# Optimization experiments

Hardware: AMD Instinct MI355X
Metric: run time of the kernel (lower is better)

## Reference

```python
import jax, jax.numpy as jnp
import numpy as np

N_NODES, N_EDGES, N_GRAPHS = 500000, 8000000, 4096
IN_SIZE, HIDDEN, OUT_SIZE = 11, 16, 4
FEAT = IN_SIZE + 7  # 18; also the (buggy) truncated sequence length in the original


def setup_inputs() -> dict:
    key = jax.random.key(0)
    ks = jax.random.split(key, 10)
    x = jax.random.normal(ks[0], (N_NODES, IN_SIZE), dtype=jnp.float32)
    edge_index = jax.random.randint(ks[1], (2, N_EDGES), 0, N_NODES)
    edge_attr = jax.random.randint(ks[2], (N_EDGES,), 0, 7)
    batch = jnp.sort(jax.random.randint(ks[3], (N_EDGES,), 0, N_GRAPHS))
    s = 0.1
    W_ih = jax.random.normal(ks[4], (4 * HIDDEN, FEAT), jnp.float32) * s
    W_hh = jax.random.normal(ks[5], (4 * HIDDEN, HIDDEN), jnp.float32) * s
    b_ih = jax.random.normal(ks[6], (4 * HIDDEN,), jnp.float32) * s
    b_hh = jax.random.normal(ks[7], (4 * HIDDEN,), jnp.float32) * s
    W_fc = jax.random.normal(ks[8], (OUT_SIZE, HIDDEN), jnp.float32) * s
    b_fc = jax.random.normal(ks[9], (OUT_SIZE,), jnp.float32) * s
    return {"x": x, "W_ih": W_ih, "W_hh": W_hh, "b_ih": b_ih, "b_hh": b_hh,
            "W_fc": W_fc, "b_fc": b_fc, "edge_index": edge_index,
            "edge_attr": edge_attr, "batch": batch, "num_graphs": N_GRAPHS}


def _forward(x, W_ih, W_hh, b_ih, b_hh, W_fc, b_fc, edge_index, edge_attr, batch, num_graphs):
    E = edge_index.shape[1]
    # Per-edge gather: node_value = x[n1] + x[n2], concat one-hot edge type (width 7)
    feat = jnp.concatenate(
        [x[edge_index[0]] + x[edge_index[1]],
         jax.nn.one_hot(edge_attr, 7, dtype=x.dtype)], axis=1)  # [E, FEAT]
    # Position of edge j within its graph: j - index of first edge of that graph
    first = jnp.searchsorted(batch, jnp.arange(num_graphs))  # [B]
    pos = jnp.arange(E) - first[batch]                        # [E], >= 0 (batch sorted)
    # Faithful to original bug: sequences truncated to first FEAT (=18) timesteps.
    # Out-of-range positions dropped by scatter mode='drop'.
    seq = jnp.zeros((num_graphs, FEAT, FEAT), x.dtype).at[batch, pos].set(feat, mode='drop')
    # Single-layer LSTM (torch gate order i, f, g, o), batch_first
    bias = b_ih + b_hh

    def step(carry, xt):
        h, c = carry
        gates = xt @ W_ih.T + h @ W_hh.T + bias  # [B, 4H]
        i, f, g, o = jnp.split(gates, 4, axis=-1)
        c = jax.nn.sigmoid(f) * c + jax.nn.sigmoid(i) * jnp.tanh(g)
        h = jax.nn.sigmoid(o) * jnp.tanh(c)
        return (h, c), None

    h0 = jnp.zeros((num_graphs, HIDDEN), x.dtype)
    (h, c), _ = jax.lax.scan(step, (h0, h0), jnp.swapaxes(seq, 0, 1))  # [T,B,F] scan
    # fc applied then last timestep taken -> equals fc(h_last)
    return h @ W_fc.T + b_fc  # [B, OUT_SIZE]


def reference(x, W_ih, W_hh, b_ih, b_hh, W_fc, b_fc, edge_index, edge_attr, batch, num_graphs):
    return _forward(x, W_ih, W_hh, b_ih, b_hh, W_fc, b_fc, edge_index, edge_attr, batch, num_graphs)
```

## Files before the change

kernel.cpp:

```cpp
#include <hip/hip_runtime.h>

#define IN_SIZE 11
#define HID 16
#define FEAT 18
#define TSTEPS 18

__device__ __forceinline__ float fast_rcp(float v) { return __builtin_amdgcn_rcpf(v); }

__device__ __forceinline__ float rl(float v, int lane) {
    return __int_as_float(__builtin_amdgcn_readlane(__float_as_int(v), lane));
}

extern "C" __global__ __launch_bounds__(256, 4)
void tgnn_lstm_fused(const float* __restrict__ x,
                     const float* __restrict__ W_ih,
                     const float* __restrict__ W_hh,
                     const float* __restrict__ b_ih,
                     const float* __restrict__ b_hh,
                     const float* __restrict__ W_fc,
                     const float* __restrict__ b_fc,
                     const int* __restrict__ edge_index,
                     const int* __restrict__ edge_attr,
                     const int* __restrict__ batch,
                     float* __restrict__ out,
                     int E, int B)
{
    const int wl  = threadIdx.x & 63;
    const int g   = (blockIdx.x * blockDim.x + threadIdx.x) >> 6;
    const int u   = wl & 15;
    const int r   = wl >> 4;
    const int row = wl;

    float wih[IN_SIZE], whh[HID];
#pragma unroll
    for (int k = 0; k < IN_SIZE; ++k) wih[k] = W_ih[row * FEAT + k];
#pragma unroll
    for (int v = 0; v < HID; ++v) whh[v] = W_hh[row * HID + v];
    const float bias = b_ih[row] + b_hh[row];
    const float wfc  = W_fc[row];
    const float bfc  = b_fc[r];

    const int tgt1 = g, tgt2 = g + 1;
    int lo1 = 0, hi1 = E, lo2 = 0, hi2 = E;
    while ((hi1 - lo1) > 64 || (hi2 - lo2) > 64) {
        const unsigned n1r = (unsigned)(hi1 - lo1);
        const unsigned n2r = (unsigned)(hi2 - lo2);
        const int p1 = lo1 + (int)((n1r * (unsigned)wl) >> 6);
        const int p2 = lo2 + (int)((n2r * (unsigned)wl) >> 6);
        const int b1 = batch[p1];
        const int b2 = batch[p2];
        const int c1 = __popcll(__ballot(b1 < tgt1));
        const int c2 = __popcll(__ballot(b2 < tgt2));
        const int nlo1 = c1 ? (lo1 + (int)((n1r * (unsigned)(c1 - 1)) >> 6) + 1) : lo1;
        const int nhi1 = (c1 < 64) ? (lo1 + (int)((n1r * (unsigned)c1) >> 6)) : hi1;
        const int nlo2 = c2 ? (lo2 + (int)((n2r * (unsigned)(c2 - 1)) >> 6) + 1) : lo2;
        const int nhi2 = (c2 < 64) ? (lo2 + (int)((n2r * (unsigned)c2) >> 6)) : hi2;
        lo1 = nlo1; hi1 = nhi1; lo2 = nlo2; hi2 = nhi2;
    }
    {
        const int n1r = hi1 - lo1, n2r = hi2 - lo2;
        int p1 = lo1 + ((wl < n1r) ? wl : 0);
        int p2 = lo2 + ((wl < n2r) ? wl : 0);
        if (p1 > E - 1) p1 = E - 1;
        if (p2 > E - 1) p2 = E - 1;
        const int b1 = batch[p1];
        const int b2 = batch[p2];
        lo1 += __popcll(__ballot((wl < n1r) && (b1 < tgt1)));
        lo2 += __popcll(__ballot((wl < n2r) && (b2 < tgt2)));
    }
    const int first = lo1;
    int cnt = lo2 - first;
    cnt = (cnt < 0) ? 0 : ((cnt > TSTEPS) ? TSTEPS : cnt);

    int n1 = 0, n2 = 0, ea = 0;
    if (wl < TSTEPS) {
        int j = first + wl;
        if (j > E - 1) j = E - 1;
        n1 = edge_index[j];
        n2 = edge_index[E + j];
        ea = edge_attr[j];
    }
    float f[IN_SIZE];
    {
        const float* xa = x + (long)n1 * IN_SIZE;
        const float* xb = x + (long)n2 * IN_SIZE;
#pragma unroll
        for (int k = 0; k < IN_SIZE; ++k) f[k] = xa[k] + xb[k];
    }
    if (wl >= cnt) {
#pragma unroll
        for (int k = 0; k < IN_SIZE; ++k) f[k] = 0.0f;
    }

    float ain[TSTEPS];
#pragma unroll
    for (int t = 0; t < TSTEPS; ++t) {
        const int eat = __builtin_amdgcn_readlane(ea, t);
        const float w1 = W_ih[row * FEAT + IN_SIZE + eat];
        float a = bias + ((t < cnt) ? w1 : 0.0f);
#pragma unroll
        for (int k = 0; k < IN_SIZE; ++k)
            a = fmaf(rl(f[k], t), wih[k], a);
        ain[t] = a;
    }

    const float sa = (r == 2) ? -2.0f : -1.0f;
    const float ma = (r == 2) ?  2.0f :  1.0f;
    const float oa = (r == 2) ? -1.0f :  0.0f;

    float h = 0.0f, c = 0.0f;
#pragma unroll
    for (int t = 0; t < TSTEPS; ++t) {
        float a;
        if (t == 0) {
            a = ain[0];
        } else {
            float A0 = ain[t], A1 = 0.0f, A2 = 0.0f, A3 = 0.0f;
#pragma unroll
            for (int v = 0; v < HID; v += 4) {
                A0 = fmaf(rl(h, v + 0), whh[v + 0], A0);
                A1 = fmaf(rl(h, v + 1), whh[v + 1], A1);
                A2 = fmaf(rl(h, v + 2), whh[v + 2], A2);
                A3 = fmaf(rl(h, v + 3), whh[v + 3], A3);
            }
            a = (A0 + A1) + (A2 + A3);
        }
        const float act = fmaf(ma, fast_rcp(1.0f + __expf(sa * a)), oa);
        const float s1 = __shfl_xor(act, 16, 64);
        const float s2 = __shfl_xor(act, 32, 64);
        const float s3 = __shfl_xor(s1, 32, 64);
        c = fmaf(s1, c, act * s2);
        const float th = fmaf(2.0f, fast_rcp(1.0f + __expf(-2.0f * c)), -1.0f);
        h = s3 * th;
    }

    const float hb = __shfl(h, u, 64);
    float p = hb * wfc;
#pragma unroll
    for (int m = 8; m >= 1; m >>= 1) p += __shfl_xor(p, m, 16);
    if (u == 0 && g < B) out[g * 4 + r] = p + bfc;
}

extern "C" void kernel_launch(void* const* d_in, const int* in_sizes, int n_in,
                              void* d_out, int out_size, void* d_ws, size_t ws_size,
                              hipStream_t stream) {
    const float* x     = (const float*)d_in[0];
    const float* W_ih  = (const float*)d_in[1];
    const float* W_hh  = (const float*)d_in[2];
    const float* b_ih  = (const float*)d_in[3];
    const float* b_hh  = (const float*)d_in[4];
    const float* W_fc  = (const float*)d_in[5];
    const float* b_fc  = (const float*)d_in[6];
    const int* edge_index = (const int*)d_in[7];
    const int* edge_attr  = (const int*)d_in[8];
    const int* batch      = (const int*)d_in[9];

    const int E = in_sizes[8];
    const int B = out_size / 4;

    const int grid = (B + 3) / 4;
    tgnn_lstm_fused<<<grid, 256, 0, stream>>>(x, W_ih, W_hh, b_ih, b_hh,
                                              W_fc, b_fc,
                                              edge_index, edge_attr, batch,
                                              (float*)d_out, E, B);
}
```

Measured before the change: 27.96 us.

## Replace per-graph binary search with full-scan boundary kernel and packed edge data

Adds a pre-pass kernel that streams the whole sorted batch array (about 32 MB), finds graph boundaries, and writes per-graph first-edge offsets plus packed edge indices and types into workspace. The LSTM kernel then reads these directly instead of running a wave-parallel binary search over batch. This removes the latency-bound search but adds a second launch and a full read of batch, which is far more traffic than the original handful of search probes.

Result: slower. 47.87 us (+71.2%).

```diff
diff --git a/kernel.cpp b/kernel.cpp
--- a/kernel.cpp
+++ b/kernel.cpp
@@ -5,25 +5,100 @@
 #define FEAT 18
 #define TSTEPS 18
 
+#define PACK_OFF 8192
+
 __device__ __forceinline__ float fast_rcp(float v) { return __builtin_amdgcn_rcpf(v); }
 
 __device__ __forceinline__ float rl(float v, int lane) {
     return __int_as_float(__builtin_amdgcn_readlane(__float_as_int(v), lane));
 }
 
+__global__ __launch_bounds__(256)
+void scan_bounds(const int* __restrict__ batch,
+                 const int* __restrict__ edge_index,
+                 const int* __restrict__ edge_attr,
+                 int* __restrict__ first_arr,
+                 int* __restrict__ pack,
+                 int E, int B)
+{
+    const int lane = threadIdx.x & 63;
+    const int nthr = gridDim.x * blockDim.x;
+    const int Q = E >> 2;
+    const int4* b4 = reinterpret_cast<const int4*>(batch);
+
+    for (int q = blockIdx.x * blockDim.x + threadIdx.x; q < Q; q += nthr) {
+        const int4 v = b4[q];
+        const int i0 = q << 2;
+        int prev = __shfl_up(v.w, 1, 64);
+        if (lane == 0) prev = (i0 == 0) ? -1 : batch[i0 - 1];
+
+        const int pa[4] = {prev, v.x, v.y, v.z};
+        const int pb[4] = {v.x,  v.y, v.z, v.w};
+#pragma unroll
+        for (int s = 0; s < 4; ++s) {
+            if (pb[s] > pa[s]) {
+                const int j0 = i0 + s;
+                for (int g = pa[s] + 1; g <= pb[s]; ++g) {
+                    first_arr[g] = j0;
+                    if (g < B) {
+                        int* pk = pack + g * 64;
+#pragma unroll
+                        for (int t = 0; t < TSTEPS; ++t) {
+                            int jj = j0 + t; if (jj > E - 1) jj = E - 1;
+                            pk[t]      = edge_index[jj];
+                            pk[18 + t] = edge_index[E + jj];
+                            pk[36 + t] = edge_attr[jj];
+                        }
+                    }
+                }
+            }
+        }
+    }
+
+    if (blockIdx.x == 0 && threadIdx.x == 0) {
+        for (int j = (Q << 2); j < E; ++j) {
+            const int a = (j == 0) ? -1 : batch[j - 1];
+            const int b = batch[j];
+            for (int g = a + 1; g <= b; ++g) {
+                first_arr[g] = j;
+                if (g < B) {
+                    int* pk = pack + g * 64;
+                    for (int t = 0; t < TSTEPS; ++t) {
+                        int jj = j + t; if (jj > E - 1) jj = E - 1;
+                        pk[t]      = edge_index[jj];
+                        pk[18 + t] = edge_index[E + jj];
+                        pk[36 + t] = edge_attr[jj];
+                    }
+                }
+            }
+        }
+        const int bl = batch[E - 1];
+        for (int g = bl + 1; g <= B; ++g) {
+            first_arr[g] = E;
+            if (g < B) {
+                int* pk = pack + g * 64;
+                for (int t = 0; t < TSTEPS; ++t) {
+                    pk[t]      = edge_index[E - 1];
+                    pk[18 + t] = edge_index[E + E - 1];
+                    pk[36 + t] = edge_attr[E - 1];
+                }
+            }
+        }
+    }
+}
+
 extern "C" __global__ __launch_bounds__(256, 4)
-void tgnn_lstm_fused(const float* __restrict__ x,
-                     const float* __restrict__ W_ih,
-                     const float* __restrict__ W_hh,
-                     const float* __restrict__ b_ih,
-                     const float* __restrict__ b_hh,
-                     const float* __restrict__ W_fc,
-                     const float* __restrict__ b_fc,
-                     const int* __restrict__ edge_index,
-                     const int* __restrict__ edge_attr,
-                     const int* __restrict__ batch,
-                     float* __restrict__ out,
-                     int E, int B)
+void tgnn_lstm_main(const float* __restrict__ x,
+                    const float* __restrict__ W_ih,
+                    const float* __restrict__ W_hh,
+                    const float* __restrict__ b_ih,
+                    const float* __restrict__ b_hh,
+                    const float* __restrict__ W_fc,
+                    const float* __restrict__ b_fc,
+                    const int* __restrict__ first_arr,
+                    const int* __restrict__ pack,
+                    float* __restrict__ out,
+                    int B)
 {
     const int wl  = threadIdx.x & 63;
     const int g   = (blockIdx.x * blockDim.x + threadIdx.x) >> 6;
@@ -40,46 +115,19 @@
     const float wfc  = W_fc[row];
     const float bfc  = b_fc[r];
 
-    const int tgt1 = g, tgt2 = g + 1;
-    int lo1 = 0, hi1 = E, lo2 = 0, hi2 = E;
-    while ((hi1 - lo1) > 64 || (hi2 - lo2) > 64) {
-        const unsigned n1r = (unsigned)(hi1 - lo1);
-        const unsigned n2r = (unsigned)(hi2 - lo2);
-        const int p1 = lo1 + (int)((n1r * (unsigned)wl) >> 6);
-        const int p2 = lo2 + (int)((n2r * (unsigned)wl) >> 6);
-        const int b1 = batch[p1];
-        const int b2 = batch[p2];
-        const int c1 = __popcll(__ballot(b1 < tgt1));
-        const int c2 = __popcll(__ballot(b2 < tgt2));
-        const int nlo1 = c1 ? (lo1 + (int)((n1r * (unsigned)(c1 - 1)) >> 6) + 1) : lo1;
-        const int nhi1 = (c1 < 64) ? (lo1 + (int)((n1r * (unsigned)c1) >> 6)) : hi1;
-        const int nlo2 = c2 ? (lo2 + (int)((n2r * (unsigned)(c2 - 1)) >> 6) + 1) : lo2;
-        const int nhi2 = (c2 < 64) ? (lo2 + (int)((n2r * (unsigned)c2) >> 6)) : hi2;
-        lo1 = nlo1; hi1 = nhi1; lo2 = nlo2; hi2 = nhi2;
-    }
-    {
-        const int n1r = hi1 - lo1, n2r = hi2 - lo2;
-        int p1 = lo1 + ((wl < n1r) ? wl : 0);
-        int p2 = lo2 + ((wl < n2r) ? wl : 0);
-        if (p1 > E - 1) p1 = E - 1;
-        if (p2 > E - 1) p2 = E - 1;
-        const int b1 = batch[p1];
-        const int b2 = batch[p2];
-        lo1 += __popcll(__ballot((wl < n1r) && (b1 < tgt1)));
-        lo2 += __popcll(__ballot((wl < n2r) && (b2 < tgt2)));
-    }
-    const int first = lo1;
-    int cnt = lo2 - first;
+    const int f0 = first_arr[g];
+    const int f1 = first_arr[g + 1];
+    int cnt = f1 - f0;
     cnt = (cnt < 0) ? 0 : ((cnt > TSTEPS) ? TSTEPS : cnt);
 
     int n1 = 0, n2 = 0, ea = 0;
     if (wl < TSTEPS) {
-        int j = first + wl;
-        if (j > E - 1) j = E - 1;
-        n1 = edge_index[j];
-        n2 = edge_index[E + j];
-        ea = edge_attr[j];
-    }
+        const int* pk = pack + g * 64;
+        n1 = pk[wl];
+        n2 = pk[18 + wl];
+        ea = pk[36 + wl];
+    }
+
     float f[IN_SIZE];
     {
         const float* xa = x + (long)n1 * IN_SIZE;
@@ -158,9 +206,14 @@
     const int E = in_sizes[8];
     const int B = out_size / 4;
 
+    int* first_arr = (int*)d_ws;
+    int* pack      = first_arr + PACK_OFF;
+
+    scan_bounds<<<2048, 256, 0, stream>>>(batch, edge_index, edge_attr,
+                                          first_arr, pack, E, B);
+
     const int grid = (B + 3) / 4;
-    tgnn_lstm_fused<<<grid, 256, 0, stream>>>(x, W_ih, W_hh, b_ih, b_hh,
-                                              W_fc, b_fc,
-                                              edge_index, edge_attr, batch,
-                                              (float*)d_out, E, B);
-}
+    tgnn_lstm_main<<<grid, 256, 0, stream>>>(x, W_ih, W_hh, b_ih, b_hh,
+                                             W_fc, b_fc, first_arr, pack,
+                                             (float*)d_out, B);
+}
```
